# Optimization experiments

Hardware: AMD Instinct MI355X
Metric: run time of the kernel (lower is better)

Reference implementation:

```python
import jax, jax.numpy as jnp
import numpy as np

D_MODEL = 1024
NUM_HEADS = 16
WINDOW = 2048  # must equal seq_len (see notes): source matmul attn(B,H,S,W) @ v(B,H,S,hd) requires W == S
SEQ_LEN = 2048
BATCH = 1


def setup_inputs() -> dict:
    key = jax.random.key(0)
    k0, k1, k2 = jax.random.split(key, 3)
    d = D_MODEL
    x = jax.random.normal(k0, (BATCH, SEQ_LEN, d), dtype=jnp.float32)
    w_qkv = jax.random.normal(k1, (3 * d, d), dtype=jnp.float32) * (d ** -0.5)
    b_qkv = jnp.zeros((3 * d,), dtype=jnp.float32)
    w_proj = jax.random.normal(k2, (d, d), dtype=jnp.float32) * (d ** -0.5)
    b_proj = jnp.zeros((d,), dtype=jnp.float32)
    return {"x": x, "w_qkv": w_qkv, "b_qkv": b_qkv, "w_proj": w_proj, "b_proj": b_proj}


def reference(x, w_qkv, b_qkv, w_proj, b_proj):
    B, S, d = x.shape
    H = NUM_HEADS
    hd = d // H
    W = WINDOW
    scale = hd ** -0.5

    # qkv projection (torch Linear: x @ W^T + b)
    qkv = x @ w_qkv.T + b_qkv                      # (B, S, 3d)
    qkv = qkv.reshape(B, S, 3, H, hd).transpose(2, 0, 3, 1, 4)  # (3, B, H, S, hd)
    q, k, v = qkv[0], qkv[1], qkv[2]

    # sliding-window scores: score[b,h,i,j] = q_i . k_padded[i+j] * scale, j in [0, W)
    pad = W // 2
    k_pad = jnp.pad(k, ((0, 0), (0, 0), (pad, pad), (0, 0)))     # (B, H, S+W, hd)
    scores_full = jnp.einsum('bhid,bhjd->bhij', q, k_pad) * scale  # (B, H, S, S+W)
    idx = jnp.arange(S)[:, None] + jnp.arange(W)[None, :]          # (S, W) banded gather indices
    scores = jnp.take_along_axis(scores_full, idx[None, None], axis=-1)  # (B, H, S, W)

    attn = jax.nn.softmax(scores, axis=-1)
    attn = jnp.nan_to_num(attn)  # faithful to torch.nan_to_num(attn, 0.0)

    # Faithful to the source: forward() does matmul(attn, v), i.e. column j of the
    # windowed attn indexes v position j directly (requires W == S).
    out = jnp.einsum('bhij,bhjd->bhid', attn, v)   # (B, H, S, hd)
    out = out.transpose(0, 2, 1, 3).reshape(B, S, d)
    out = out @ w_proj.T + b_proj
    return out, attn
```

## Files before the change

### kernel.cpp

```cpp
#include <hip/hip_runtime.h>
#include <hip/hip_bf16.h>

typedef __hip_bfloat16 bf16;
typedef __attribute__((ext_vector_type(8))) short short8;
typedef __attribute__((ext_vector_type(4))) float f32x4;

#define DEV static __device__ __forceinline__

static constexpr int SEQ = 2048;
static constexpr int DM  = 1024;
static constexpr int NH  = 16;
static constexpr int HD  = 64;
static constexpr int WIN = 2048;
static constexpr int PAD = 1024;

DEV void async16(const void* g, void* l) {
  __builtin_amdgcn_global_load_lds(
      (__attribute__((address_space(1))) void*)(g),
      (__attribute__((address_space(3))) void*)(l), 16, 0, 0);
}

__global__ __launch_bounds__(256) void k_cvt(const float* __restrict__ x,
                                             const float* __restrict__ wq,
                                             const float* __restrict__ wp,
                                             bf16* __restrict__ xb,
                                             bf16* __restrict__ wqb,
                                             bf16* __restrict__ wpb) {
  const int NX = SEQ * DM, NQ = 3 * DM * DM, NP = DM * DM;
  const int tot = (NX + NQ + NP) >> 2;
  const int stride = gridDim.x * 256;
  for (int i = blockIdx.x * 256 + threadIdx.x; i < tot; i += stride) {
    int e = i << 2;
    const float* s; bf16* d; int o;
    if (e < NX)            { s = x;  d = xb;  o = e; }
    else if (e < NX + NQ)  { s = wq; d = wqb; o = e - NX; }
    else                   { s = wp; d = wpb; o = e - NX - NQ; }
    float4 v = *(const float4*)(s + o);
    __align__(8) bf16 t4[4] = {__float2bfloat16(v.x), __float2bfloat16(v.y),
                               __float2bfloat16(v.z), __float2bfloat16(v.w)};
    *(uint2*)(d + o) = *(uint2*)t4;
  }
}

DEV void gemm_core(const bf16* __restrict__ A, const bf16* __restrict__ B,
                   int m0, int n0, int K, int tid, bf16* As, bf16* Bs,
                   f32x4 (&acc)[4][4]) {
  const int lane = tid & 63, wid = tid >> 6;
  const int wm = wid >> 1, wn = wid & 1;
  const int l15 = lane & 15, l4 = lane >> 4;
  for (int k0 = 0; k0 < K; k0 += 64) {
    __syncthreads();
    #pragma unroll
    for (int it = 0; it < 4; ++it) {
      int rb = it * 32 + wid * 8;
      int r  = rb + (lane >> 3);
      int c  = (lane & 7) * 8;
      async16(A + (size_t)(m0 + r) * K + k0 + c, As + rb * 64);
      async16(B + (size_t)(n0 + r) * K + k0 + c, Bs + rb * 64);
    }
    asm volatile("s_waitcnt vmcnt(0)" ::: "memory");
    __syncthreads();
    #pragma unroll
    for (int kk = 0; kk < 2; ++kk) {
      short8 a[4], b[4];
      #pragma unroll
      for (int im = 0; im < 4; ++im)
        a[im] = *(const short8*)(As + (wm * 64 + im * 16 + l15) * 64 + kk * 32 + l4 * 8);
      #pragma unroll
      for (int in = 0; in < 4; ++in)
        b[in] = *(const short8*)(Bs + (wn * 64 + in * 16 + l15) * 64 + kk * 32 + l4 * 8);
      #pragma unroll
      for (int im = 0; im < 4; ++im)
        #pragma unroll
        for (int in = 0; in < 4; ++in)
          acc[im][in] = __builtin_amdgcn_mfma_f32_16x16x32_bf16(a[im], b[in], acc[im][in], 0, 0, 0);
    }
  }
}

__global__ __launch_bounds__(256) void k_gemm_qkv(const bf16* __restrict__ A,
                                                  const bf16* __restrict__ B,
                                                  const float* __restrict__ bias,
                                                  bf16* __restrict__ qo,
                                                  bf16* __restrict__ ko,
                                                  bf16* __restrict__ vt) {
  __shared__ bf16 As[128 * 64], Bs[128 * 64];
  const int tid = threadIdx.x, lane = tid & 63;
  const int wid = tid >> 6, wm = wid >> 1, wn = wid & 1;
  const int l15 = lane & 15, l4 = lane >> 4;
  const int m0 = blockIdx.x * 128, n0 = blockIdx.y * 128;
  f32x4 acc[4][4] = {};
  gemm_core(A, B, m0, n0, DM, tid, As, Bs, acc);
  #pragma unroll
  for (int im = 0; im < 4; ++im)
    #pragma unroll
    for (int in = 0; in < 4; ++in) {
      int col = n0 + wn * 64 + in * 16 + l15;
      float bval = bias[col];
      int t = col >> 10, h = (col >> 6) & 15, dd = col & 63;
      int row0 = m0 + wm * 64 + im * 16 + l4 * 4;
      if (t == 2) {
        __align__(8) bf16 t4[4];
        #pragma unroll
        for (int r = 0; r < 4; ++r)
          t4[r] = __float2bfloat16(acc[im][in][r] + bval);
        *(uint2*)&vt[((size_t)h * HD + dd) * SEQ + row0] = *(uint2*)t4;
      } else {
        #pragma unroll
        for (int r = 0; r < 4; ++r) {
          float v = acc[im][in][r] + bval;
          size_t idx = ((size_t)h * SEQ + row0 + r) * HD + dd;
          if (t == 0) qo[idx] = __float2bfloat16(v * 0.18033688011112042f);
          else        ko[idx] = __float2bfloat16(v);
        }
      }
    }
}

DEV void stage_kp(const bf16* kbase, int i0, int tt, int lane, bf16* dst) {
  #pragma unroll
  for (int it = 0; it < 4; ++it) {
    int r  = it * 8 + (lane >> 3);
    int cg = lane & 7;
    int jp = i0 + tt * 32 + r;
    int krow = jp - PAD;
    krow = krow < 0 ? 0 : (krow > SEQ - 1 ? SEQ - 1 : krow);
    int sc = (cg ^ (r & 7)) * 8;
    async16(kbase + (size_t)krow * HD + sc, dst + it * 8 * 64);
  }
}

DEV void qk_mfma_lds(const bf16* KPb, const short8 (&qf)[2][2], int l15, int l4,
                     f32x4 (&sf)[2][2]) {
  __builtin_amdgcn_s_setprio(1);
  #pragma unroll
  for (int kg = 0; kg < 2; ++kg) {
    short8 kfr[2];
    #pragma unroll
    for (int fn = 0; fn < 2; ++fn) {
      int jl = fn * 16 + l15;
      int pg = (kg * 4 + l4) ^ (jl & 7);
      kfr[fn] = *(const short8*)&KPb[jl * 64 + pg * 8];
    }
    #pragma unroll
    for (int fm = 0; fm < 2; ++fm)
      #pragma unroll
      for (int fn = 0; fn < 2; ++fn)
        sf[fm][fn] = __builtin_amdgcn_mfma_f32_16x16x32_bf16(qf[fm][kg], kfr[fn], sf[fm][fn], 0, 0, 0);
  }
  __builtin_amdgcn_s_setprio(0);
}

DEV void qk_mfma_lds_sw(const bf16* KPb, const short8 (&qf)[2][2], int l15, int l4,
                        f32x4 (&sf)[2][2]) {
  __builtin_amdgcn_s_setprio(1);
  #pragma unroll
  for (int kg = 0; kg < 2; ++kg) {
    short8 kfr[2];
    #pragma unroll
    for (int fj = 0; fj < 2; ++fj) {
      int jl = fj * 16 + l15;
      int pg = (kg * 4 + l4) ^ (jl & 7);
      kfr[fj] = *(const short8*)&KPb[jl * 64 + pg * 8];
    }
    #pragma unroll
    for (int fj = 0; fj < 2; ++fj)
      #pragma unroll
      for (int fi = 0; fi < 2; ++fi)
        sf[fj][fi] = __builtin_amdgcn_mfma_f32_16x16x32_bf16(kfr[fj], qf[fi][kg], sf[fj][fi], 0, 0, 0);
  }
  __builtin_amdgcn_s_setprio(0);
}

DEV int pad_lo(int i0) { int d = PAD - i0; return d <= 0 ? 0 : (d >> 5); }
DEV int pad_hi(int i0) { int t = ((PAD + SEQ - 1 - i0) >> 5) + 1; return t > 65 ? 65 : t; }

__global__ __launch_bounds__(256) void k_attn1(const bf16* __restrict__ q,
                                               const bf16* __restrict__ kkk,
                                               float* __restrict__ psums) {
  const int h  = blockIdx.x >> 6;
  const int i0 = (blockIdx.x & 63) << 5;
  const int tid = threadIdx.x;
  const int c = tid >> 6;
  const int lane = tid & 63;
  const int l15 = lane & 15, l4 = lane >> 4;

  __shared__ bf16 KP[4][2][32 * 64];

  constexpr int st[5] = {0, 16, 32, 48, 65};
  const int lo_g = pad_lo(i0), hi_g = pad_hi(i0);
  int lo = st[c] > lo_g ? st[c] : lo_g;
  int hi = st[c + 1] < hi_g ? st[c + 1] : hi_g;

  short8 qf[2][2];
  #pragma unroll
  for (int fi = 0; fi < 2; ++fi)
    #pragma unroll
    for (int kg = 0; kg < 2; ++kg)
      qf[fi][kg] = *(const short8*)&q[((size_t)h * SEQ + i0 + fi * 16 + l15) * HD + kg * 32 + l4 * 8];

  const bf16* kbase = kkk + (size_t)h * SEQ * HD;

  float psum[2] = {0.f, 0.f};
  if (lo < hi) {
    stage_kp(kbase, i0, lo, lane, KP[c][lo & 1]);
    for (int tt = lo; tt < hi; ++tt) {
      int nxt = (tt + 1 < hi) ? tt + 1 : tt;
      stage_kp(kbase, i0, nxt, lane, KP[c][(tt + 1) & 1]);
      asm volatile("s_waitcnt vmcnt(4)" ::: "memory");
      f32x4 sf[2][2] = {};
      qk_mfma_lds_sw(KP[c][tt & 1], qf, l15, l4, sf);
      const bool interior = (tt >= 1) && (tt <= 63) &&
                            (i0 + tt * 32 >= PAD) && (i0 + tt * 32 + 31 < PAD + SEQ);
      if (interior) {
        #pragma unroll
        for (int fj = 0; fj < 2; ++fj)
          #pragma unroll
          for (int r = 0; r < 4; ++r) {
            psum[0] += __builtin_amdgcn_exp2f(sf[fj][0][r]);
            psum[1] += __builtin_amdgcn_exp2f(sf[fj][1][r]);
          }
      } else {
        #pragma unroll
        for (int fj = 0; fj < 2; ++fj)
          #pragma unroll
          for (int r = 0; r < 4; ++r) {
            int jj = tt * 32 + fj * 16 + l4 * 4 + r;
            int jp = i0 + jj;
            bool pad = (jp < PAD) || (jp >= PAD + SEQ);
            #pragma unroll
            for (int fi = 0; fi < 2; ++fi) {
              int iloc = fi * 16 + l15;
              float e = pad ? 1.0f : __builtin_amdgcn_exp2f(sf[fj][fi][r]);
              if ((unsigned)(jj - iloc) < (unsigned)WIN) psum[fi] += e;
            }
          }
      }
    }
  }
  float r0 = psum[0];
  r0 += __shfl_xor(r0, 16); r0 += __shfl_xor(r0, 32);
  float r1 = psum[1];
  r1 += __shfl_xor(r1, 16); r1 += __shfl_xor(r1, 32);
  if (lane < 32) {
    int i_abs = i0 + lane;
    float s = (lane < 16) ? r0 : r1;
    if (c == 0) {
      int cl = i0 + lo_g * 32 - i_abs; if (cl < 0) cl = 0;
      int cr = i_abs + WIN - (i0 + hi_g * 32); if (cr < 0) cr = 0;
      s += (float)(cl + cr);
    }
    psums[((size_t)c * NH + h) * SEQ + i_abs] = s;
  }
}

__global__ __launch_bounds__(256) void k_attn2(const bf16* __restrict__ q,
                                               const bf16* __restrict__ kkk,
                                               const bf16* __restrict__ vT,
                                               const float* __restrict__ psums,
                                               float* __restrict__ attn,
                                               bf16* __restrict__ ao) {
  const int h  = blockIdx.x >> 6;
  const int i0 = (blockIdx.x & 63) << 5;
  const int tid = threadIdx.x;
  const int c = tid >> 6;
  const int lane = tid & 63;
  const int l15 = lane & 15, l4 = lane >> 4;
  const int c0 = c * 16, c1 = c0 + 16;
  const int lo_g = pad_lo(i0), hi_g = pad_hi(i0);

  __shared__ bf16 KP[4][2][32 * 64];
  __shared__ float JF[4][32 * 64];

  float inv[2][4];
  #pragma unroll
  for (int fm = 0; fm < 2; ++fm)
    #pragma unroll
    for (int r = 0; r < 4; ++r) {
      int row = i0 + fm * 16 + l4 * 4 + r;
      float s = 0.f;
      #pragma unroll
      for (int cc = 0; cc < 4; ++cc)
        s += psums[((size_t)cc * NH + h) * SEQ + row];
      inv[fm][r] = __builtin_amdgcn_rcpf(s);
    }

  short8 qf[2][2];
  #pragma unroll
  for (int fm = 0; fm < 2; ++fm)
    #pragma unroll
    for (int kg = 0; kg < 2; ++kg)
      qf[fm][kg] = *(const short8*)&q[((size_t)h * SEQ + i0 + fm * 16 + l15) * HD + kg * 32 + l4 * 8];

  const bf16* kbase = kkk + (size_t)h * SEQ * HD;
  const bf16* vbase = vT + (size_t)h * HD * SEQ;
  float* abase = attn + (size_t)(h * SEQ + i0) * WIN;
  float* JFW = JF[c];

  f32x4 oacc[2][4] = {};
  stage_kp(kbase, i0, c0, lane, KP[c][0]);
  for (int tt = c0; tt <= c1; ++tt) {
    short8 bv[4];
    if (tt > c0) {
      int jb = (tt - 1) * 32;
      #pragma unroll
      for (int nd = 0; nd < 4; ++nd)
        bv[nd] = *(const short8*)&vbase[(size_t)(nd * 16 + l15) * SEQ + jb + l4 * 8];
    }
    int nxt = (tt < c1) ? tt + 1 : tt;
    stage_kp(kbase, i0, nxt, lane, KP[c][(tt + 1) & 1]);
    if (tt == c0)          asm volatile("s_waitcnt vmcnt(4)" ::: "memory");
    else if (tt == c0 + 1) asm volatile("s_waitcnt vmcnt(8)" ::: "memory");
    else                   asm volatile("s_waitcnt vmcnt(12)" ::: "memory");

    const bool fp = (tt < lo_g) || (tt >= hi_g);
    f32x4 sf[2][2] = {};
    if (!fp) qk_mfma_lds(KP[c][tt & 1], qf, l15, l4, sf);

    const bool allv = (i0 + tt * 32 >= PAD) && (i0 + tt * 32 + 31 < PAD + SEQ);
    #pragma unroll
    for (int fm = 0; fm < 2; ++fm)
      #pragma unroll
      for (int fn = 0; fn < 2; ++fn) {
        int J0 = tt * 32 + fn * 16 + l15;
        bool padc = fp || (!allv && ((i0 + J0 < PAD) || (i0 + J0 >= PAD + SEQ)));
        #pragma unroll
        for (int r = 0; r < 4; ++r) {
          int row = fm * 16 + l4 * 4 + r;
          float e = padc ? 1.0f : __builtin_amdgcn_exp2f(sf[fm][fn][r]);
          float val = e * inv[fm][r];
          int j6 = (J0 - row) & 63;
          int pgrp = (j6 >> 2) ^ ((row & 7) << 1);
          JFW[row * 64 + pgrp * 4 + (j6 & 3)] = val;
        }
      }

    if (tt > c0) {
      const int g = (tt - 1) & 1;
      const int Jb = (tt - 1) * 32;
      #pragma unroll
      for (int s = 0; s < 4; ++s) {
        int row = s * 8 + (lane >> 3);
        int c8 = lane & 7;
        int pgrp = (g * 8 + c8) ^ ((row & 7) << 1);
        f32x4 vv = *(const f32x4*)&JFW[row * 64 + pgrp * 4];
        __builtin_nontemporal_store(vv, (f32x4*)(abase + (size_t)row * WIN + Jb + c8 * 4));
      }
      short8 af[2];
      #pragma unroll
      for (int fm = 0; fm < 2; ++fm) {
        int row = fm * 16 + l15;
        int pg0 = (g * 8 + l4 * 2) ^ ((row & 7) << 1);
        const float* p = &JFW[row * 64 + pg0 * 4];
        union { unsigned short u[8]; short8 v; } tmp;
        #pragma unroll
        for (int e = 0; e < 8; ++e)
          tmp.u[e] = __bfloat16_as_ushort(__float2bfloat16(p[e]));
        af[fm] = tmp.v;
      }
      __builtin_amdgcn_s_setprio(1);
      #pragma unroll
      for (int fm = 0; fm < 2; ++fm)
        #pragma unroll
        for (int nd = 0; nd < 4; ++nd)
          oacc[fm][nd] = __builtin_amdgcn_mfma_f32_16x16x32_bf16(af[fm], bv[nd], oacc[fm][nd], 0, 0, 0);
      __builtin_amdgcn_s_setprio(0);
    }
  }

  #pragma unroll
  for (int fm = 0; fm < 2; ++fm)
    #pragma unroll
    for (int nd = 0; nd < 4; ++nd)
      #pragma unroll
      for (int r = 0; r < 4; ++r)
        JFW[(fm * 16 + l4 * 4 + r) * 64 + nd * 16 + l15] = oacc[fm][nd][r];
  __syncthreads();
  {
    int row = tid >> 3;
    int d0 = (tid & 7) * 8;
    const float* j0p = &JF[0][0];
    union { unsigned short u[8]; short8 v; } o;
    #pragma unroll
    for (int e = 0; e < 8; ++e) {
      int idx = row * 64 + d0 + e;
      float s = j0p[idx] + j0p[2048 + idx] + j0p[4096 + idx] + j0p[6144 + idx];
      o.u[e] = __bfloat16_as_ushort(__float2bfloat16(s));
    }
    *(short8*)&ao[(size_t)(i0 + row) * DM + h * HD + d0] = o.v;
  }
}

__global__ __launch_bounds__(256) void k_gemm_proj(const bf16* __restrict__ A,
                                                   const bf16* __restrict__ B,
                                                   const float* __restrict__ bias,
                                                   float* __restrict__ out) {
  __shared__ bf16 As[128 * 64], Bs[128 * 64];
  const int tid = threadIdx.x, lane = tid & 63;
  const int wid = tid >> 6, wm = wid >> 1, wn = wid & 1;
  const int l15 = lane & 15, l4 = lane >> 4;
  const int m0 = blockIdx.x * 128, n0 = blockIdx.y * 128;
  f32x4 acc[4][4] = {};
  gemm_core(A, B, m0, n0, DM, tid, As, Bs, acc);
  #pragma unroll
  for (int im = 0; im < 4; ++im)
    #pragma unroll
    for (int in = 0; in < 4; ++in) {
      int col = n0 + wn * 64 + in * 16 + l15;
      float bval = bias[col];
      #pragma unroll
      for (int r = 0; r < 4; ++r) {
        int row = m0 + wm * 64 + im * 16 + l4 * 4 + r;
        out[(size_t)row * DM + col] = acc[im][in][r] + bval;
      }
    }
}

extern "C" void kernel_launch(void* const* d_in, const int* in_sizes, int n_in,
                              void* d_out, int out_size, void* d_ws, size_t ws_size,
                              hipStream_t stream) {
  (void)in_sizes; (void)n_in; (void)out_size; (void)ws_size;
  const float* x  = (const float*)d_in[0];
  const float* wq = (const float*)d_in[1];
  const float* bq = (const float*)d_in[2];
  const float* wp = (const float*)d_in[3];
  const float* bp = (const float*)d_in[4];
  float* out  = (float*)d_out;
  float* attn = out + (size_t)SEQ * DM;

  char* ws = (char*)d_ws;
  bf16* xb    = (bf16*)(ws + (size_t) 0);
  bf16* wqb   = (bf16*)(ws + ((size_t)4  << 20));
  bf16* wpb   = (bf16*)(ws + ((size_t)10 << 20));
  bf16* qarr  = (bf16*)(ws + ((size_t)12 << 20));
  bf16* karr  = (bf16*)(ws + ((size_t)16 << 20));
  bf16* vt    = (bf16*)(ws + ((size_t)24 << 20));
  bf16* ao    = (bf16*)(ws + ((size_t)28 << 20));
  float* psums= (float*)(ws + ((size_t)8 << 20));

  k_cvt<<<dim3(1024), dim3(256), 0, stream>>>(x, wq, wp, xb, wqb, wpb);
  k_gemm_qkv<<<dim3(16, 24), dim3(256), 0, stream>>>(xb, wqb, bq, qarr, karr, vt);
  k_attn1<<<dim3(1024), dim3(256), 0, stream>>>(qarr, karr, psums);
  k_attn2<<<dim3(1024), dim3(256), 0, stream>>>(qarr, karr, vt, psums, attn, ao);
  k_gemm_proj<<<dim3(16, 8), dim3(256), 0, stream>>>(ao, wpb, bp, out);
}
```

Baseline: 152.1 us.

## Fuse softmax row-sum pass into attention kernel and stage probabilities as bf16

Merges the two attention kernels into one, so each block first computes the softmax row sums, reduces them through shared memory and then runs the normalised write-out and PV pass. This removes one kernel launch, the global psums round trip and the reload of Q. Unnormalised exponentials are now staged in LDS as bf16 instead of fp32 and scaled by 1/sum when read, and the PV output is normalised at the end. This halves LDS staging, but the stored attn values carry bf16 rounding before normalisation.

```diff
diff --git a/kernel.cpp b/kernel.cpp
--- a/kernel.cpp
+++ b/kernel.cpp
@@ -4,6 +4,7 @@
 typedef __hip_bfloat16 bf16;
 typedef __attribute__((ext_vector_type(8))) short short8;
 typedef __attribute__((ext_vector_type(4))) float f32x4;
+typedef __attribute__((ext_vector_type(4))) unsigned short ushort4v;
 
 #define DEV static __device__ __forceinline__
 
@@ -175,115 +176,23 @@
 DEV int pad_lo(int i0) { int d = PAD - i0; return d <= 0 ? 0 : (d >> 5); }
 DEV int pad_hi(int i0) { int t = ((PAD + SEQ - 1 - i0) >> 5) + 1; return t > 65 ? 65 : t; }
 
-__global__ __launch_bounds__(256) void k_attn1(const bf16* __restrict__ q,
-                                               const bf16* __restrict__ kkk,
-                                               float* __restrict__ psums) {
+__global__ __launch_bounds__(256) void k_attn(const bf16* __restrict__ q,
+                                              const bf16* __restrict__ kkk,
+                                              const bf16* __restrict__ vT,
+                                              float* __restrict__ attn,
+                                              bf16* __restrict__ ao) {
   const int h  = blockIdx.x >> 6;
   const int i0 = (blockIdx.x & 63) << 5;
   const int tid = threadIdx.x;
   const int c = tid >> 6;
   const int lane = tid & 63;
   const int l15 = lane & 15, l4 = lane >> 4;
+  const int lo_g = pad_lo(i0), hi_g = pad_hi(i0);
 
   __shared__ bf16 KP[4][2][32 * 64];
-
-  constexpr int st[5] = {0, 16, 32, 48, 65};
-  const int lo_g = pad_lo(i0), hi_g = pad_hi(i0);
-  int lo = st[c] > lo_g ? st[c] : lo_g;
-  int hi = st[c + 1] < hi_g ? st[c + 1] : hi_g;
-
-  short8 qf[2][2];
-  #pragma unroll
-  for (int fi = 0; fi < 2; ++fi)
-    #pragma unroll
-    for (int kg = 0; kg < 2; ++kg)
-      qf[fi][kg] = *(const short8*)&q[((size_t)h * SEQ + i0 + fi * 16 + l15) * HD + kg * 32 + l4 * 8];
-
-  const bf16* kbase = kkk + (size_t)h * SEQ * HD;
-
-  float psum[2] = {0.f, 0.f};
-  if (lo < hi) {
-    stage_kp(kbase, i0, lo, lane, KP[c][lo & 1]);
-    for (int tt = lo; tt < hi; ++tt) {
-      int nxt = (tt + 1 < hi) ? tt + 1 : tt;
-      stage_kp(kbase, i0, nxt, lane, KP[c][(tt + 1) & 1]);
-      asm volatile("s_waitcnt vmcnt(4)" ::: "memory");
-      f32x4 sf[2][2] = {};
-      qk_mfma_lds_sw(KP[c][tt & 1], qf, l15, l4, sf);
-      const bool interior = (tt >= 1) && (tt <= 63) &&
-                            (i0 + tt * 32 >= PAD) && (i0 + tt * 32 + 31 < PAD + SEQ);
-      if (interior) {
-        #pragma unroll
-        for (int fj = 0; fj < 2; ++fj)
-          #pragma unroll
-          for (int r = 0; r < 4; ++r) {
-            psum[0] += __builtin_amdgcn_exp2f(sf[fj][0][r]);
-            psum[1] += __builtin_amdgcn_exp2f(sf[fj][1][r]);
-          }
-      } else {
-        #pragma unroll
-        for (int fj = 0; fj < 2; ++fj)
-          #pragma unroll
-          for (int r = 0; r < 4; ++r) {
-            int jj = tt * 32 + fj * 16 + l4 * 4 + r;
-            int jp = i0 + jj;
-            bool pad = (jp < PAD) || (jp >= PAD + SEQ);
-            #pragma unroll
-            for (int fi = 0; fi < 2; ++fi) {
-              int iloc = fi * 16 + l15;
-              float e = pad ? 1.0f : __builtin_amdgcn_exp2f(sf[fj][fi][r]);
-              if ((unsigned)(jj - iloc) < (unsigned)WIN) psum[fi] += e;
-            }
-          }
-      }
-    }
-  }
-  float r0 = psum[0];
-  r0 += __shfl_xor(r0, 16); r0 += __shfl_xor(r0, 32);
-  float r1 = psum[1];
-  r1 += __shfl_xor(r1, 16); r1 += __shfl_xor(r1, 32);
-  if (lane < 32) {
-    int i_abs = i0 + lane;
-    float s = (lane < 16) ? r0 : r1;
-    if (c == 0) {
-      int cl = i0 + lo_g * 32 - i_abs; if (cl < 0) cl = 0;
-      int cr = i_abs + WIN - (i0 + hi_g * 32); if (cr < 0) cr = 0;
-      s += (float)(cl + cr);
-    }
-    psums[((size_t)c * NH + h) * SEQ + i_abs] = s;
-  }
-}
-
-__global__ __launch_bounds__(256) void k_attn2(const bf16* __restrict__ q,
-                                               const bf16* __restrict__ kkk,
-                                               const bf16* __restrict__ vT,
-                                               const float* __restrict__ psums,
-                                               float* __restrict__ attn,
-                                               bf16* __restrict__ ao) {
-  const int h  = blockIdx.x >> 6;
-  const int i0 = (blockIdx.x & 63) << 5;
-  const int tid = threadIdx.x;
-  const int c = tid >> 6;
-  const int lane = tid & 63;
-  const int l15 = lane & 15, l4 = lane >> 4;
-  const int c0 = c * 16, c1 = c0 + 16;
-  const int lo_g = pad_lo(i0), hi_g = pad_hi(i0);
-
-  __shared__ bf16 KP[4][2][32 * 64];
-  __shared__ float JF[4][32 * 64];
-
-  float inv[2][4];
-  #pragma unroll
-  for (int fm = 0; fm < 2; ++fm)
-    #pragma unroll
-    for (int r = 0; r < 4; ++r) {
-      int row = i0 + fm * 16 + l4 * 4 + r;
-      float s = 0.f;
-      #pragma unroll
-      for (int cc = 0; cc < 4; ++cc)
-        s += psums[((size_t)cc * NH + h) * SEQ + row];
-      inv[fm][r] = __builtin_amdgcn_rcpf(s);
-    }
+  __shared__ unsigned short JFB[4][32 * 64];
+  __shared__ float sums[4][32];
+  __shared__ float invL[32];
 
   short8 qf[2][2];
   #pragma unroll
@@ -295,8 +204,76 @@
   const bf16* kbase = kkk + (size_t)h * SEQ * HD;
   const bf16* vbase = vT + (size_t)h * HD * SEQ;
   float* abase = attn + (size_t)(h * SEQ + i0) * WIN;
-  float* JFW = JF[c];
-
+
+  {
+    constexpr int st[5] = {0, 16, 32, 48, 65};
+    int lo = st[c] > lo_g ? st[c] : lo_g;
+    int hi = st[c + 1] < hi_g ? st[c + 1] : hi_g;
+
+    float psum[2] = {0.f, 0.f};
+    if (lo < hi) {
+      stage_kp(kbase, i0, lo, lane, KP[c][lo & 1]);
+      for (int tt = lo; tt < hi; ++tt) {
+        int nxt = (tt + 1 < hi) ? tt + 1 : tt;
+        stage_kp(kbase, i0, nxt, lane, KP[c][(tt + 1) & 1]);
+        asm volatile("s_waitcnt vmcnt(4)" ::: "memory");
+        f32x4 sf[2][2] = {};
+        qk_mfma_lds_sw(KP[c][tt & 1], qf, l15, l4, sf);
+        const bool interior = (tt >= 1) && (tt <= 63) &&
+                              (i0 + tt * 32 >= PAD) && (i0 + tt * 32 + 31 < PAD + SEQ);
+        if (interior) {
+          #pragma unroll
+          for (int fj = 0; fj < 2; ++fj)
+            #pragma unroll
+            for (int r = 0; r < 4; ++r) {
+              psum[0] += __builtin_amdgcn_exp2f(sf[fj][0][r]);
+              psum[1] += __builtin_amdgcn_exp2f(sf[fj][1][r]);
+            }
+        } else {
+          #pragma unroll
+          for (int fj = 0; fj < 2; ++fj)
+            #pragma unroll
+            for (int r = 0; r < 4; ++r) {
+              int jj = tt * 32 + fj * 16 + l4 * 4 + r;
+              int jp = i0 + jj;
+              bool pad = (jp < PAD) || (jp >= PAD + SEQ);
+              #pragma unroll
+              for (int fi = 0; fi < 2; ++fi) {
+                int iloc = fi * 16 + l15;
+                float e = pad ? 1.0f : __builtin_amdgcn_exp2f(sf[fj][fi][r]);
+                if ((unsigned)(jj - iloc) < (unsigned)WIN) psum[fi] += e;
+              }
+            }
+        }
+      }
+    }
+    float r0 = psum[0];
+    r0 += __shfl_xor(r0, 16); r0 += __shfl_xor(r0, 32);
+    float r1 = psum[1];
+    r1 += __shfl_xor(r1, 16); r1 += __shfl_xor(r1, 32);
+    if (lane < 32) {
+      int i_abs = i0 + lane;
+      float s = (lane < 16) ? r0 : r1;
+      if (c == 0) {
+        int cl = i0 + lo_g * 32 - i_abs; if (cl < 0) cl = 0;
+        int cr = i_abs + WIN - (i0 + hi_g * 32); if (cr < 0) cr = 0;
+        s += (float)(cl + cr);
+      }
+      sums[c][lane] = s;
+    }
+  }
+  __syncthreads();
+  if (tid < 32)
+    invL[tid] = __builtin_amdgcn_rcpf(sums[0][tid] + sums[1][tid] +
+                                      sums[2][tid] + sums[3][tid]);
+  __syncthreads();
+
+  float invf[4];
+  #pragma unroll
+  for (int s2 = 0; s2 < 4; ++s2) invf[s2] = invL[s2 * 8 + (lane >> 3)];
+
+  const int c0 = c * 16, c1 = c0 + 16;
+  unsigned short* JW = JFB[c];
   f32x4 oacc[2][4] = {};
   stage_kp(kbase, i0, c0, lane, KP[c][0]);
   for (int tt = c0; tt <= c1; ++tt) {
@@ -328,35 +305,33 @@
         for (int r = 0; r < 4; ++r) {
           int row = fm * 16 + l4 * 4 + r;
           float e = padc ? 1.0f : __builtin_amdgcn_exp2f(sf[fm][fn][r]);
-          float val = e * inv[fm][r];
           int j6 = (J0 - row) & 63;
-          int pgrp = (j6 >> 2) ^ ((row & 7) << 1);
-          JFW[row * 64 + pgrp * 4 + (j6 & 3)] = val;
+          int sg = (j6 >> 3) ^ (row & 7);
+          JW[row * 64 + sg * 8 + (j6 & 7)] = __bfloat16_as_ushort(__float2bfloat16(e));
         }
       }
 
     if (tt > c0) {
       const int g = (tt - 1) & 1;
       const int Jb = (tt - 1) * 32;
-      #pragma unroll
-      for (int s = 0; s < 4; ++s) {
-        int row = s * 8 + (lane >> 3);
-        int c8 = lane & 7;
-        int pgrp = (g * 8 + c8) ^ ((row & 7) << 1);
-        f32x4 vv = *(const f32x4*)&JFW[row * 64 + pgrp * 4];
+      const int c8 = lane & 7;
+      #pragma unroll
+      for (int s2 = 0; s2 < 4; ++s2) {
+        int row = s2 * 8 + (lane >> 3);
+        int sg = (g * 4 + (c8 >> 1)) ^ (row & 7);
+        ushort4v uv = *(const ushort4v*)&JW[row * 64 + sg * 8 + (c8 & 1) * 4];
+        f32x4 vv;
+        #pragma unroll
+        for (int e = 0; e < 4; ++e)
+          vv[e] = __uint_as_float((unsigned)uv[e] << 16) * invf[s2];
         __builtin_nontemporal_store(vv, (f32x4*)(abase + (size_t)row * WIN + Jb + c8 * 4));
       }
       short8 af[2];
       #pragma unroll
       for (int fm = 0; fm < 2; ++fm) {
         int row = fm * 16 + l15;
-        int pg0 = (g * 8 + l4 * 2) ^ ((row & 7) << 1);
-        const float* p = &JFW[row * 64 + pg0 * 4];
-        union { unsigned short u[8]; short8 v; } tmp;
-        #pragma unroll
-        for (int e = 0; e < 8; ++e)
-          tmp.u[e] = __bfloat16_as_ushort(__float2bfloat16(p[e]));
-        af[fm] = tmp.v;
+        int sg = (g * 4 + l4) ^ (row & 7);
+        af[fm] = *(const short8*)&JW[row * 64 + sg * 8];
       }
       __builtin_amdgcn_s_setprio(1);
       #pragma unroll
@@ -368,23 +343,26 @@
     }
   }
 
+  __syncthreads();
+  float* OX = (float*)&KP[0][0][0];
+  float* OW = OX + c * 2048;
   #pragma unroll
   for (int fm = 0; fm < 2; ++fm)
     #pragma unroll
     for (int nd = 0; nd < 4; ++nd)
       #pragma unroll
       for (int r = 0; r < 4; ++r)
-        JFW[(fm * 16 + l4 * 4 + r) * 64 + nd * 16 + l15] = oacc[fm][nd][r];
+        OW[(fm * 16 + l4 * 4 + r) * 64 + nd * 16 + l15] = oacc[fm][nd][r];
   __syncthreads();
   {
     int row = tid >> 3;
     int d0 = (tid & 7) * 8;
-    const float* j0p = &JF[0][0];
+    float iv = invL[row];
     union { unsigned short u[8]; short8 v; } o;
     #pragma unroll
     for (int e = 0; e < 8; ++e) {
       int idx = row * 64 + d0 + e;
-      float s = j0p[idx] + j0p[2048 + idx] + j0p[4096 + idx] + j0p[6144 + idx];
+      float s = (OX[idx] + OX[2048 + idx] + OX[4096 + idx] + OX[6144 + idx]) * iv;
       o.u[e] = __bfloat16_as_ushort(__float2bfloat16(s));
     }
     *(short8*)&ao[(size_t)(i0 + row) * DM + h * HD + d0] = o.v;
@@ -436,11 +414,9 @@
   bf16* karr  = (bf16*)(ws + ((size_t)16 << 20));
   bf16* vt    = (bf16*)(ws + ((size_t)24 << 20));
   bf16* ao    = (bf16*)(ws + ((size_t)28 << 20));
-  float* psums= (float*)(ws + ((size_t)8 << 20));
 
   k_cvt<<<dim3(1024), dim3(256), 0, stream>>>(x, wq, wp, xb, wqb, wpb);
   k_gemm_qkv<<<dim3(16, 24), dim3(256), 0, stream>>>(xb, wqb, bq, qarr, karr, vt);
-  k_attn1<<<dim3(1024), dim3(256), 0, stream>>>(qarr, karr, psums);
-  k_attn2<<<dim3(1024), dim3(256), 0, stream>>>(qarr, karr, vt, psums, attn, ao);
+  k_attn<<<dim3(1024), dim3(256), 0, stream>>>(qarr, karr, vt, attn, ao);
   k_gemm_proj<<<dim3(16, 8), dim3(256), 0, stream>>>(ao, wpb, bp, out);
 }
```

New measurement: 150.5 us. Within noise of the previous version (-1.1%).
